# Kernel optimization log

Hardware: AMD Instinct MI355X
Metric: run time of the kernel (lower is better)

Reference implementation:

```python
import jax, jax.numpy as jnp
import numpy as np

NEG_INF = -1000000000.0  # matches torch masked_fill constant


def setup_inputs() -> dict:
    key = jax.random.key(0)
    k1, k2, k3, k4 = jax.random.split(key, 4)
    B, H, S, D = 4, 16, 2048, 64
    q = jax.random.normal(k1, (B, H, S, D), dtype=jnp.float32)
    k = jax.random.normal(k2, (B, H, S, D), dtype=jnp.float32)
    v = jax.random.normal(k3, (B, H, S, D), dtype=jnp.float32)
    mask = jax.random.randint(k4, (B, 1, S, S), 0, 2, dtype=jnp.int32)
    return {"q": q, "k": k, "v": v, "mask": mask}


def reference(q, k, v, mask):
    d_k = q.shape[-1]
    scale = 1.0 / jnp.sqrt(jnp.asarray(d_k, dtype=q.dtype))
    # scores: [B,H,S,S]
    scores = jnp.einsum("bhqd,bhkd->bhqk", q, k) * scale
    scores = jnp.where(mask == 0, jnp.asarray(NEG_INF, dtype=scores.dtype), scores)
    p_attn = jax.nn.softmax(scores, axis=-1)
    return jnp.einsum("bhqk,bhkd->bhqd", p_attn, v)
```

## Files before the change

kernel.cpp:

```cpp
#include <hip/hip_runtime.h>

#define S_LEN 2048
#define DHEAD 64
#define NWORDS (4 * S_LEN * (S_LEN / 64))
#define KV_TILES 32
#define NHEADS 64
#define TILE_SHORTS 4096

typedef __attribute__((ext_vector_type(4))) float f32x4;
typedef __attribute__((ext_vector_type(4))) int i32x4;
typedef __attribute__((ext_vector_type(8))) short short8v;
typedef __attribute__((ext_vector_type(4))) short short4v;

static __device__ __forceinline__ short f2bf(float x) {
  unsigned u = __float_as_uint(x);
  u += 0x7fffu + ((u >> 16) & 1u);
  return (short)(u >> 16);
}

static __device__ __forceinline__ void mfma16(const i32x4& a, const i32x4& b, f32x4& c) {
  asm("v_mfma_f32_16x16x32_bf16 %0, %1, %2, %0" : "+v"(c) : "v"(a), "v"(b));
}

static __device__ __forceinline__ int pack_bf16_rtz(float hi, float lo) {
  return (int)__builtin_amdgcn_perm(__float_as_uint(hi), __float_as_uint(lo), 0x07060302u);
}

static __device__ __forceinline__ void gload_lds16(const void* g, void* l) {
  __builtin_amdgcn_global_load_lds((const __attribute__((address_space(1))) void*)g,
                                   (__attribute__((address_space(3))) void*)l, 16, 0, 0);
}

__global__ __launch_bounds__(256) void preprocess_kernel(
    const float* __restrict__ k, const float* __restrict__ v, const int* __restrict__ mask,
    short* __restrict__ kswz, short* __restrict__ vswz, unsigned long long* __restrict__ mpack) {
  const int blk = blockIdx.x, tid = threadIdx.x;
  if (blk < 2048) {
    const float* kb = k + (size_t)blk * 64 * DHEAD;
    short* dst = kswz + (size_t)blk * TILE_SHORTS;
#pragma unroll
    for (int it = 0; it < 2; ++it) {
      int g = tid + it * 256;
      int r = g >> 3, c = g & 7;
      const f32x4* src = (const f32x4*)(kb + r * DHEAD + c * 8);
      f32x4 a = src[0], d2 = src[1];
      short8v w;
#pragma unroll
      for (int i = 0; i < 4; ++i) w[i] = f2bf(a[i]);
#pragma unroll
      for (int i = 0; i < 4; ++i) w[4 + i] = f2bf(d2[i]);
      *(short8v*)&dst[r * 64 + ((c ^ (r & 7)) << 3)] = w;
    }
  } else if (blk < 4096) {
    const int t = blk - 2048;
    const float* vb = v + (size_t)t * 64 * DHEAD;
    short* dst = vswz + (size_t)t * TILE_SHORTS;
#pragma unroll
    for (int it = 0; it < 2; ++it) {
      int dcol = tid & 63;
      int kc = (tid >> 6) + it * 4;
      short8v w;
#pragma unroll
      for (int i = 0; i < 8; ++i) w[i] = f2bf(vb[(size_t)(kc * 8 + i) * DHEAD + dcol]);
      *(short8v*)&dst[dcol * 64 + ((kc ^ (dcol & 7)) << 3)] = w;
    }
  } else {
    const int t = blk - 4096;
    const int lane = tid & 63;
    for (int w = t * 256 + (tid >> 6); w < t * 256 + 256; w += 4) {
      int m = mask[(size_t)w * 64 + lane];
      unsigned long long bits = __ballot(m != 0);
      if (lane == 0) mpack[w] = bits;
    }
  }
}

__global__ __launch_bounds__(512) void attn_fast_kernel(
    const float* __restrict__ q, const short* __restrict__ kswz, const short* __restrict__ vswz,
    const unsigned long long* __restrict__ mpack, float* __restrict__ out) {
  __shared__ __align__(16) short Klds[2][TILE_SHORTS];
  __shared__ __align__(16) short Vlds[2][TILE_SHORTS];
  __shared__ __align__(16) short Plds[8][1024];

  const int tid = threadIdx.x, lane = tid & 63, wave = tid >> 6;
  const int l15 = lane & 15, l4 = lane >> 4;

  const int id = blockIdx.x;
  const int work = (id & 7) * 64 + (id >> 3);
  const int head = work >> 3;
  const int qb = (work & 7) * 256;
  const int b = head >> 4;

  const float* qbase = q + ((size_t)head * S_LEN + qb + wave * 32) * DHEAD;
  float* obase = out + ((size_t)head * S_LEN + qb + wave * 32) * DHEAD;
  const short* ktiles = kswz + (size_t)head * KV_TILES * TILE_SHORTS;
  const short* vtiles = vswz + (size_t)head * KV_TILES * TILE_SHORTS;

  const float QSC = 0.125f;
  i32x4 qfrag[2][2];
#pragma unroll
  for (int qt = 0; qt < 2; ++qt) {
    const float* qp = qbase + (size_t)(qt * 16 + l15) * DHEAD + l4 * 8;
#pragma unroll
    for (int ch = 0; ch < 2; ++ch) {
      const f32x4* p = (const f32x4*)(qp + ch * 32);
      f32x4 a = p[0], c = p[1];
      short t[8];
#pragma unroll
      for (int i = 0; i < 4; ++i) t[i] = f2bf(a[i] * QSC);
#pragma unroll
      for (int i = 0; i < 4; ++i) t[4 + i] = f2bf(c[i] * QSC);
      i32x4 w;
#pragma unroll
      for (int i = 0; i < 4; ++i)
        w[i] = (int)((unsigned short)t[2 * i] | ((unsigned)(unsigned short)t[2 * i + 1] << 16));
      qfrag[qt][ch] = w;
    }
  }

  const unsigned long long* mprow[2];
#pragma unroll
  for (int qt = 0; qt < 2; ++qt)
    mprow[qt] = mpack + ((size_t)b * S_LEN + qb + wave * 32 + qt * 16 + l15) * KV_TILES;

  float l_run[2] = {0.f, 0.f};
  f32x4 oacc[2][4];
#pragma unroll
  for (int qt = 0; qt < 2; ++qt)
#pragma unroll
    for (int dt = 0; dt < 4; ++dt) oacc[qt][dt] = f32x4{0.f, 0.f, 0.f, 0.f};

  auto stage = [&](int buf, int kb) {
    const short* kg = ktiles + (size_t)kb * TILE_SHORTS + tid * 8;
    const short* vg = vtiles + (size_t)kb * TILE_SHORTS + tid * 8;
    gload_lds16(kg, &Klds[buf][tid * 8]);
    gload_lds16(vg, &Vlds[buf][tid * 8]);
  };

  stage(0, 0);
  __syncthreads();
  int cur = 0;

  for (int kb = 0; kb < KV_TILES; ++kb) {
    if (kb + 1 < KV_TILES) stage(cur ^ 1, kb + 1);
    unsigned long long mw[2];
#pragma unroll
    for (int qt = 0; qt < 2; ++qt) mw[qt] = mprow[qt][kb];

    f32x4 acc[2][4];
#pragma unroll
    for (int qt = 0; qt < 2; ++qt)
#pragma unroll
      for (int kt = 0; kt < 4; ++kt) acc[qt][kt] = f32x4{0.f, 0.f, 0.f, 0.f};
    __builtin_amdgcn_s_setprio(1);
#pragma unroll
    for (int kt = 0; kt < 4; ++kt) {
      int krow = kt * 16 + l15;
#pragma unroll
      for (int ch = 0; ch < 2; ++ch) {
        i32x4 kf = *(const i32x4*)&Klds[cur][krow * 64 + (((ch * 4 + l4) ^ (krow & 7)) << 3)];
        mfma16(kf, qfrag[0][ch], acc[0][kt]);
        mfma16(kf, qfrag[1][ch], acc[1][kt]);
      }
    }
    __builtin_amdgcn_s_setprio(0);

    i32x4 pa[2][2];
#pragma unroll
    for (int qt = 0; qt < 2; ++qt) {
      float p[16], ps = 0.f;
#pragma unroll
      for (int kt = 0; kt < 4; ++kt) {
        unsigned bits = (unsigned)(mw[qt] >> (kt * 16 + l4 * 4)) & 0xFu;
#pragma unroll
        for (int r = 0; r < 4; ++r) {
          float e = __expf(acc[qt][kt][r]);
          p[kt * 4 + r] = ((bits >> r) & 1u) ? e : 0.f;
          ps += p[kt * 4 + r];
        }
      }
      ps += __shfl_xor(ps, 16);
      ps += __shfl_xor(ps, 32);
      l_run[qt] += ps;

#pragma unroll
      for (int kt = 0; kt < 4; ++kt) {
        int2 wv;
        wv.x = pack_bf16_rtz(p[kt * 4 + 1], p[kt * 4 + 0]);
        wv.y = pack_bf16_rtz(p[kt * 4 + 3], p[kt * 4 + 2]);
        int col = kt * 16 + l4 * 4;
        *(int2*)&Plds[wave][l15 * 64 + (((col >> 3) ^ (l15 & 7)) << 3) + (col & 7)] = wv;
      }
#pragma unroll
      for (int ch = 0; ch < 2; ++ch)
        pa[qt][ch] = *(const i32x4*)&Plds[wave][l15 * 64 + (((ch * 4 + l4) ^ (l15 & 7)) << 3)];
    }

    __builtin_amdgcn_s_setprio(1);
#pragma unroll
    for (int dt = 0; dt < 4; ++dt) {
      int drow = dt * 16 + l15;
#pragma unroll
      for (int ch = 0; ch < 2; ++ch) {
        i32x4 vf = *(const i32x4*)&Vlds[cur][drow * 64 + (((ch * 4 + l4) ^ (drow & 7)) << 3)];
        mfma16(pa[0][ch], vf, oacc[0][dt]);
        mfma16(pa[1][ch], vf, oacc[1][dt]);
      }
    }
    __builtin_amdgcn_s_setprio(0);
    __syncthreads();
    cur ^= 1;
  }

#pragma unroll
  for (int qt = 0; qt < 2; ++qt)
#pragma unroll
    for (int r = 0; r < 4; ++r) {
      float inv = 1.f / __shfl(l_run[qt], l4 * 4 + r);
      float* op = obase + (size_t)(qt * 16 + l4 * 4 + r) * DHEAD + l15;
#pragma unroll
      for (int dt = 0; dt < 4; ++dt) op[dt * 16] = oacc[qt][dt][r] * inv;
    }
}

__global__ __launch_bounds__(256) void attn_fallback_kernel(
    const float* __restrict__ q, const float* __restrict__ k, const float* __restrict__ v,
    const int* __restrict__ mraw, float* __restrict__ out) {
  __shared__ short Klds[64 * 64];
  __shared__ short Vtlds[64 * 64];
  __shared__ short Plds[4][16 * 64];

  const int tid = threadIdx.x, lane = tid & 63, wave = tid >> 6;
  const int l15 = lane & 15, l4 = lane >> 4;
  const int id = blockIdx.x;
  const int work = (id & 7) * 256 + (id >> 3);
  const int head = work >> 5;
  const int qb = (work & 31) * 64;
  const int b = head >> 4;

  const float* qbase = q + ((size_t)head * S_LEN + qb) * DHEAD;
  const float* kbase = k + (size_t)head * S_LEN * DHEAD;
  const float* vbase = v + (size_t)head * S_LEN * DHEAD;
  float* obase = out + ((size_t)head * S_LEN + qb) * DHEAD;
  const int qrow_w = wave * 16 + l15;

  i32x4 qfrag[2];
  {
    const float* qp = qbase + (size_t)qrow_w * DHEAD + l4 * 8;
#pragma unroll
    for (int ch = 0; ch < 2; ++ch) {
      const f32x4* p = (const f32x4*)(qp + ch * 32);
      f32x4 a = p[0], c = p[1];
      short t[8];
#pragma unroll
      for (int i = 0; i < 4; ++i) t[i] = f2bf(a[i] * 0.125f);
#pragma unroll
      for (int i = 0; i < 4; ++i) t[4 + i] = f2bf(c[i] * 0.125f);
      i32x4 w;
#pragma unroll
      for (int i = 0; i < 4; ++i)
        w[i] = (int)((unsigned short)t[2 * i] | ((unsigned)(unsigned short)t[2 * i + 1] << 16));
      qfrag[ch] = w;
    }
  }
  const int* mrrow = mraw + ((size_t)b * S_LEN + qb + qrow_w) * S_LEN;

  float m_run = -INFINITY, l_run = 0.f;
  f32x4 oacc[4] = {f32x4{0,0,0,0}, f32x4{0,0,0,0}, f32x4{0,0,0,0}, f32x4{0,0,0,0}};

  for (int kb = 0; kb < KV_TILES; ++kb) {
#pragma unroll
    for (int it = 0; it < 2; ++it) {
      int g = tid + it * 256;
      int r = g >> 3, c = g & 7;
      const f32x4* src = (const f32x4*)(kbase + (size_t)(kb * 64 + r) * DHEAD + c * 8);
      f32x4 a = src[0], d2 = src[1];
      short8v w;
#pragma unroll
      for (int i = 0; i < 4; ++i) w[i] = f2bf(a[i]);
#pragma unroll
      for (int i = 0; i < 4; ++i) w[4 + i] = f2bf(d2[i]);
      *(short8v*)&Klds[r * 64 + ((c ^ (r & 7)) << 3)] = w;
    }
#pragma unroll
    for (int it = 0; it < 2; ++it) {
      int dcol = tid & 63;
      int kc = (tid >> 6) + it * 4;
      short8v w;
#pragma unroll
      for (int i = 0; i < 8; ++i) w[i] = f2bf(vbase[(size_t)(kb * 64 + kc * 8 + i) * DHEAD + dcol]);
      *(short8v*)&Vtlds[dcol * 64 + ((kc ^ (dcol & 7)) << 3)] = w;
    }
    __syncthreads();

    float sc[16];
#pragma unroll
    for (int kt = 0; kt < 4; ++kt) {
      f32x4 acc = {0.f, 0.f, 0.f, 0.f};
      int krow = kt * 16 + l15;
#pragma unroll
      for (int ch = 0; ch < 2; ++ch) {
        i32x4 af = *(const i32x4*)&Klds[krow * 64 + (((ch * 4 + l4) ^ (krow & 7)) << 3)];
        mfma16(af, qfrag[ch], acc);
      }
      i32x4 mv = *(const i32x4*)(mrrow + kb * 64 + kt * 16 + l4 * 4);
      unsigned bits = (mv[0] != 0 ? 1u : 0u) | (mv[1] != 0 ? 2u : 0u) |
                      (mv[2] != 0 ? 4u : 0u) | (mv[3] != 0 ? 8u : 0u);
#pragma unroll
      for (int r = 0; r < 4; ++r) sc[kt * 4 + r] = ((bits >> r) & 1u) ? acc[r] : -1e9f;
    }

    float mb = sc[0];
#pragma unroll
    for (int i = 1; i < 16; ++i) mb = fmaxf(mb, sc[i]);
    mb = fmaxf(mb, __shfl_xor(mb, 16));
    mb = fmaxf(mb, __shfl_xor(mb, 32));
    float mnew = fmaxf(m_run, mb);
    float alpha = __expf(m_run - mnew);
    float p[16], ps = 0.f;
#pragma unroll
    for (int i = 0; i < 16; ++i) { p[i] = __expf(sc[i] - mnew); ps += p[i]; }
    ps += __shfl_xor(ps, 16);
    ps += __shfl_xor(ps, 32);
    l_run = l_run * alpha + ps;
    m_run = mnew;
#pragma unroll
    for (int r = 0; r < 4; ++r) {
      float ar = __shfl(alpha, l4 * 4 + r);
#pragma unroll
      for (int dt = 0; dt < 4; ++dt) oacc[dt][r] *= ar;
    }
#pragma unroll
    for (int kt = 0; kt < 4; ++kt) {
      short4v w;
#pragma unroll
      for (int r = 0; r < 4; ++r) w[r] = f2bf(p[kt * 4 + r]);
      int col = kt * 16 + l4 * 4;
      *(short4v*)&Plds[wave][l15 * 64 + (((col >> 3) ^ (l15 & 7)) << 3) + (col & 7)] = w;
    }
    i32x4 pa[2];
#pragma unroll
    for (int ch = 0; ch < 2; ++ch)
      pa[ch] = *(const i32x4*)&Plds[wave][l15 * 64 + (((ch * 4 + l4) ^ (l15 & 7)) << 3)];
#pragma unroll
    for (int dt = 0; dt < 4; ++dt) {
      int drow = dt * 16 + l15;
#pragma unroll
      for (int ch = 0; ch < 2; ++ch) {
        i32x4 bf = *(const i32x4*)&Vtlds[drow * 64 + (((ch * 4 + l4) ^ (drow & 7)) << 3)];
        mfma16(pa[ch], bf, oacc[dt]);
      }
    }
    __syncthreads();
  }
#pragma unroll
  for (int r = 0; r < 4; ++r) {
    float inv = 1.f / __shfl(l_run, l4 * 4 + r);
    float* op = obase + (size_t)(wave * 16 + l4 * 4 + r) * DHEAD + l15;
#pragma unroll
    for (int dt = 0; dt < 4; ++dt) op[dt * 16] = oacc[dt][r] * inv;
  }
}

extern "C" void kernel_launch(void* const* d_in, const int* in_sizes, int n_in,
                              void* d_out, int out_size, void* d_ws, size_t ws_size,
                              hipStream_t stream) {
  const float* q = (const float*)d_in[0];
  const float* k = (const float*)d_in[1];
  const float* v = (const float*)d_in[2];
  const int* mask = (const int*)d_in[3];
  float* out = (float*)d_out;

  const size_t mask_bytes = (size_t)NWORDS * 8;
  const size_t kv_bytes = (size_t)NHEADS * KV_TILES * TILE_SHORTS * 2;
  if (ws_size >= mask_bytes + 2 * kv_bytes) {
    unsigned long long* mp = (unsigned long long*)d_ws;
    short* kswz = (short*)((char*)d_ws + mask_bytes);
    short* vswz = (short*)((char*)d_ws + mask_bytes + kv_bytes);
    preprocess_kernel<<<5120, 256, 0, stream>>>(k, v, mask, kswz, vswz, mp);
    attn_fast_kernel<<<512, 512, 0, stream>>>(q, kswz, vswz, mp, out);
  } else {
    attn_fallback_kernel<<<2048, 256, 0, stream>>>(q, k, v, mask, out);
  }
}
```

Measured before the change: 179.7 us.

## Prefetch mask words, defer row-sum reduction, interleave PV MMA per query tile

The mask bit-words for the next KV tile are now loaded one iteration ahead, alongside the K/V staging, so the global load latency overlaps with compute. The cross-lane shuffle reduction of the softmax row sum moves out of the loop and runs once at the end on per-lane partial sums. The P·V MFMAs for each query tile now run right after that tile's P is written and read back from LDS, instead of after both tiles. This is meant to cut per-iteration latency and shuffle overhead, at the cost of reading V fragments from LDS twice per iteration and slightly higher register pressure.

```diff
diff --git a/kernel.cpp b/kernel.cpp
--- a/kernel.cpp
+++ b/kernel.cpp
@@ -123,7 +123,7 @@
   for (int qt = 0; qt < 2; ++qt)
     mprow[qt] = mpack + ((size_t)b * S_LEN + qb + wave * 32 + qt * 16 + l15) * KV_TILES;
 
-  float l_run[2] = {0.f, 0.f};
+  float l_part[2] = {0.f, 0.f};
   f32x4 oacc[2][4];
 #pragma unroll
   for (int qt = 0; qt < 2; ++qt)
@@ -138,14 +138,17 @@
   };
 
   stage(0, 0);
+  unsigned long long mw_cur[2] = {mprow[0][0], mprow[1][0]};
   __syncthreads();
   int cur = 0;
 
   for (int kb = 0; kb < KV_TILES; ++kb) {
-    if (kb + 1 < KV_TILES) stage(cur ^ 1, kb + 1);
-    unsigned long long mw[2];
-#pragma unroll
-    for (int qt = 0; qt < 2; ++qt) mw[qt] = mprow[qt][kb];
+    unsigned long long mw_nxt[2] = {0ull, 0ull};
+    if (kb + 1 < KV_TILES) {
+      stage(cur ^ 1, kb + 1);
+      mw_nxt[0] = mprow[0][kb + 1];
+      mw_nxt[1] = mprow[1][kb + 1];
+    }
 
     f32x4 acc[2][4];
 #pragma unroll
@@ -165,13 +168,12 @@
     }
     __builtin_amdgcn_s_setprio(0);
 
-    i32x4 pa[2][2];
 #pragma unroll
     for (int qt = 0; qt < 2; ++qt) {
       float p[16], ps = 0.f;
 #pragma unroll
       for (int kt = 0; kt < 4; ++kt) {
-        unsigned bits = (unsigned)(mw[qt] >> (kt * 16 + l4 * 4)) & 0xFu;
+        unsigned bits = (unsigned)(mw_cur[qt] >> (kt * 16 + l4 * 4)) & 0xFu;
 #pragma unroll
         for (int r = 0; r < 4; ++r) {
           float e = __expf(acc[qt][kt][r]);
@@ -179,9 +181,7 @@
           ps += p[kt * 4 + r];
         }
       }
-      ps += __shfl_xor(ps, 16);
-      ps += __shfl_xor(ps, 32);
-      l_run[qt] += ps;
+      l_part[qt] += ps;
 
 #pragma unroll
       for (int kt = 0; kt < 4; ++kt) {
@@ -191,32 +191,44 @@
         int col = kt * 16 + l4 * 4;
         *(int2*)&Plds[wave][l15 * 64 + (((col >> 3) ^ (l15 & 7)) << 3) + (col & 7)] = wv;
       }
+      i32x4 pa[2];
 #pragma unroll
       for (int ch = 0; ch < 2; ++ch)
-        pa[qt][ch] = *(const i32x4*)&Plds[wave][l15 * 64 + (((ch * 4 + l4) ^ (l15 & 7)) << 3)];
-    }
-
-    __builtin_amdgcn_s_setprio(1);
-#pragma unroll
-    for (int dt = 0; dt < 4; ++dt) {
-      int drow = dt * 16 + l15;
-#pragma unroll
-      for (int ch = 0; ch < 2; ++ch) {
-        i32x4 vf = *(const i32x4*)&Vlds[cur][drow * 64 + (((ch * 4 + l4) ^ (drow & 7)) << 3)];
-        mfma16(pa[0][ch], vf, oacc[0][dt]);
-        mfma16(pa[1][ch], vf, oacc[1][dt]);
-      }
-    }
-    __builtin_amdgcn_s_setprio(0);
+        pa[ch] = *(const i32x4*)&Plds[wave][l15 * 64 + (((ch * 4 + l4) ^ (l15 & 7)) << 3)];
+
+      __builtin_amdgcn_s_setprio(1);
+#pragma unroll
+      for (int dt = 0; dt < 4; ++dt) {
+        int drow = dt * 16 + l15;
+#pragma unroll
+        for (int ch = 0; ch < 2; ++ch) {
+          i32x4 vf = *(const i32x4*)&Vlds[cur][drow * 64 + (((ch * 4 + l4) ^ (drow & 7)) << 3)];
+          mfma16(pa[ch], vf, oacc[qt][dt]);
+        }
+      }
+      __builtin_amdgcn_s_setprio(0);
+    }
+
     __syncthreads();
     cur ^= 1;
+    mw_cur[0] = mw_nxt[0];
+    mw_cur[1] = mw_nxt[1];
+  }
+
+  float l_red[2];
+#pragma unroll
+  for (int qt = 0; qt < 2; ++qt) {
+    float s = l_part[qt];
+    s += __shfl_xor(s, 16);
+    s += __shfl_xor(s, 32);
+    l_red[qt] = s;
   }
 
 #pragma unroll
   for (int qt = 0; qt < 2; ++qt)
 #pragma unroll
     for (int r = 0; r < 4; ++r) {
-      float inv = 1.f / __shfl(l_run[qt], l4 * 4 + r);
+      float inv = 1.f / __shfl(l_red[qt], l4 * 4 + r);
       float* op = obase + (size_t)(qt * 16 + l4 * 4 + r) * DHEAD + l15;
 #pragma unroll
       for (int dt = 0; dt < 4; ++dt) op[dt * 16] = oacc[qt][dt][r] * inv;
```

Measured after the change: 187.2 us. 4.2% more time.
